# Optimization experiments

Hardware: AMD Instinct MI355X
Metric: run time of the kernel (lower is better)

Reference implementation:

```python
import jax, jax.numpy as jnp
import numpy as np

D_MODEL = 256
D_STATE = 64
D_CONV = 4
EXPAND = 2
HEADDIM = 64
D_INNER = EXPAND * D_MODEL            # 512
NHEADS = D_INNER // HEADDIM           # 8
D_XBC = D_INNER + 2 * D_STATE         # 640 (x, B, C; ngroups=1)
D_IN_PROJ = 2 * D_INNER + 2 * D_STATE + NHEADS  # 1160


def setup_inputs() -> dict:
    key = jax.random.key(0)
    ks = jax.random.split(key, 8)
    x = jax.random.normal(ks[0], (64, 5000, 12), jnp.float32)
    W_in = jax.random.normal(ks[1], (D_MODEL, D_IN_PROJ), jnp.float32) * 0.02
    conv_w = jax.random.normal(ks[2], (D_XBC, D_CONV), jnp.float32) * 0.1
    conv_b = jnp.zeros((D_XBC,), jnp.float32)
    A_log = jnp.log(jax.random.uniform(ks[3], (NHEADS,), jnp.float32, 1.0, 16.0))
    dt_bias = jax.random.normal(ks[4], (NHEADS,), jnp.float32) * 0.1
    D = jnp.ones((NHEADS,), jnp.float32)
    norm_w = jnp.ones((D_INNER,), jnp.float32)
    W_out = jax.random.normal(ks[5], (D_INNER, D_MODEL), jnp.float32) * 0.02
    return {"x": x, "W_in": W_in, "conv_w": conv_w, "conv_b": conv_b,
            "A_log": A_log, "dt_bias": dt_bias, "D": D,
            "norm_w": norm_w, "W_out": W_out}


def _mamba2(u, W_in, conv_w, conv_b, A_log, dt_bias, D, norm_w, W_out):
    b, l, _ = u.shape
    zxbcdt = u @ W_in                                   # (b,l,1160)
    z = zxbcdt[..., :D_INNER]                           # (b,l,512)
    xBC = zxbcdt[..., D_INNER:D_INNER + D_XBC]          # (b,l,640)
    dt = zxbcdt[..., D_INNER + D_XBC:]                  # (b,l,8)
    # causal depthwise conv1d (kernel 4) + SiLU
    xp = jnp.pad(xBC, ((0, 0), (D_CONV - 1, 0), (0, 0)))
    xBC = sum(xp[:, k:k + l, :] * conv_w[:, k] for k in range(D_CONV)) + conv_b
    xBC = jax.nn.silu(xBC)
    xs = xBC[..., :D_INNER].reshape(b, l, NHEADS, HEADDIM)
    Bm = xBC[..., D_INNER:D_INNER + D_STATE]            # (b,l,64)
    Cm = xBC[..., D_INNER + D_STATE:]                   # (b,l,64)
    dt = jax.nn.softplus(dt + dt_bias)                  # (b,l,h)
    A = -jnp.exp(A_log)                                 # (h,)

    def step(h, inp):
        x_t, dt_t, B_t, C_t = inp                       # (b,h,p),(b,h),(b,n),(b,n)
        decay = jnp.exp(dt_t * A)                       # (b,h)
        h = h * decay[..., None, None] + (dt_t[..., None] * x_t)[..., None] * B_t[:, None, None, :]
        y = jnp.einsum('bhpn,bn->bhp', h, C_t)
        return h, y

    h0 = jnp.zeros((b, NHEADS, HEADDIM, D_STATE), u.dtype)
    _, ys = jax.lax.scan(step, h0, (xs.transpose(1, 0, 2, 3), dt.transpose(1, 0, 2),
                                    Bm.transpose(1, 0, 2), Cm.transpose(1, 0, 2)))
    y = ys.transpose(1, 0, 2, 3) + D[None, None, :, None] * xs   # D skip, per head
    y = y.reshape(b, l, D_INNER)
    # RMSNormGated: gate then rmsnorm
    y = y * jax.nn.silu(z)
    y = y * jax.lax.rsqrt(jnp.mean(y * y, axis=-1, keepdims=True) + 1e-5) * norm_w
    return y @ W_out                                    # (b,l,256)


def reference(x, W_in, conv_w, conv_b, A_log, dt_bias, D, norm_w, W_out):
    b = x.shape[0]
    u = x.reshape(b, 250, 240)                          # 'b (t p1) f -> b t (p1 f)'
    u = jnp.pad(u, ((0, 0), (0, 0), (0, D_MODEL - 240)))
    y = _mamba2(u, W_in, conv_w, conv_b, A_log, dt_bias, D, norm_w, W_out)
    y = jax.nn.selu(y)                                  # AlphaDropout is identity at eval
    y = y[..., :240]
    return y.reshape(b, 5000, 12)
```

## Files before the change

kernel.cpp:

```cpp
#include <hip/hip_runtime.h>
#include <cstdint>
#include <cstddef>

#define D_MODEL 256
#define D_STATE 64
#define HEADDIM 64
#define D_INNER 512
#define NHEADS 8
#define D_XBC 640
#define NPROJ 1160
#define ZXW 1152
#define BATCH 64
#define SEQ 250
#define ROWS (BATCH * SEQ)
#define KIN 240
#define KPAD 256
#define NPAD 1280
#define TPAD 256

typedef __bf16 bf16x8 __attribute__((ext_vector_type(8)));
typedef float f32x4 __attribute__((ext_vector_type(4)));

typedef __attribute__((address_space(1))) const void gv_t;
typedef __attribute__((address_space(3))) void lv_t;

__device__ __forceinline__ float readlane_f(float v, int lane) {
    return __uint_as_float(__builtin_amdgcn_readlane(__float_as_uint(v), lane));
}
__device__ __forceinline__ float silu_f(float x) { return x * (1.f / (1.f + __expf(-x))); }
__device__ __forceinline__ unsigned short bf16_rne(float f) {
    unsigned int u = __float_as_uint(f);
    u += 0x7fff + ((u >> 16) & 1);
    return (unsigned short)(u >> 16);
}
__device__ __forceinline__ float bf2f(unsigned short u) {
    return __uint_as_float(((unsigned int)u) << 16);
}
__device__ __forceinline__ unsigned int pack2(float a, float b) {
    return (unsigned int)bf16_rne(a) | ((unsigned int)bf16_rne(b) << 16);
}

#define NA (ROWS * KPAD)
#define NB (NPAD * KPAD)
#define NW (D_MODEL * D_INNER)
__global__ __launch_bounds__(256) void cast_all_kernel(const float* __restrict__ x,
                                                       const float* __restrict__ Win,
                                                       const float* __restrict__ Wout,
                                                       unsigned short* __restrict__ a_bf,
                                                       unsigned short* __restrict__ bt_bf,
                                                       unsigned short* __restrict__ wt_bf) {
    int idx = blockIdx.x * 256 + threadIdx.x;
    if (idx < NA) {
        int row = idx >> 8, c = idx & 255;
        float v = (c < KIN) ? x[row * KIN + c] : 0.f;
        a_bf[idx] = bf16_rne(v);
    } else if (idx < NA + NB) {
        int r = idx - NA;
        int n = r >> 8, k = r & 255;
        float v = (n < NPROJ && k < KIN) ? Win[k * NPROJ + n] : 0.f;
        bt_bf[r] = bf16_rne(v);
    } else if (idx < NA + NB + NW) {
        int r = idx - NA - NB;
        int n = r & 255, k = r >> 8;
        wt_bf[n * D_INNER + k] = bf16_rne(Wout[k * D_MODEL + n]);
    }
}

__global__ __launch_bounds__(256) void gemm1_mfma(const unsigned short* __restrict__ A,
                                                  const unsigned short* __restrict__ Bt,
                                                  const float* __restrict__ dt_bias,
                                                  unsigned short* __restrict__ Czx,
                                                  float* __restrict__ dtp) {
    __shared__ unsigned short As[128 * 32];
    __shared__ unsigned short Bs[128 * 32];
    const int tid = threadIdx.x;
    const int lane = tid & 63, wave = tid >> 6;
    const int wm = wave >> 1, wn = wave & 1;
    const int q = lane >> 4, l15 = lane & 15;
    const int lin = blockIdx.y * 10 + blockIdx.x;
    const int xcd = lin & 7, rank = lin >> 3;
    const int newid = (xcd < 2 ? xcd * 157 : 2 * 157 + (xcd - 2) * 156) + rank;
    const int by = newid / 10, bx = newid - by * 10;
    const int rowBase = by * 128, colBase = bx * 128;
    f32x4 acc[4][4] = {};

    const int sr = tid >> 2;
    const int sc = (tid & 3) * 8;

    const unsigned short* gA = A + (size_t)(rowBase + sr) * KPAD + sc;
    const unsigned short* gB = Bt + (size_t)(colBase + sr) * KPAD + sc;
    unsigned short* lA = &As[sr * 32 + sc];
    unsigned short* lB = &Bs[sr * 32 + sc];

    for (int k0 = 0; k0 < KPAD; k0 += 32) {
        __builtin_amdgcn_global_load_lds((gv_t*)(gA + k0), (lv_t*)lA, 16, 0, 0);
        __builtin_amdgcn_global_load_lds((gv_t*)(gA + 64 * KPAD + k0),
                                         (lv_t*)(lA + 64 * 32), 16, 0, 0);
        __builtin_amdgcn_global_load_lds((gv_t*)(gB + k0), (lv_t*)lB, 16, 0, 0);
        __builtin_amdgcn_global_load_lds((gv_t*)(gB + 64 * KPAD + k0),
                                         (lv_t*)(lB + 64 * 32), 16, 0, 0);
        __syncthreads();

        bf16x8 bfr[4];
#pragma unroll
        for (int nt = 0; nt < 4; nt++)
            bfr[nt] = *(const bf16x8*)&Bs[(wn * 64 + nt * 16 + l15) * 32 + q * 8];
#pragma unroll
        for (int mt = 0; mt < 4; mt++) {
            bf16x8 afr = *(const bf16x8*)&As[(wm * 64 + mt * 16 + l15) * 32 + q * 8];
#pragma unroll
            for (int nt = 0; nt < 4; nt++)
                acc[mt][nt] = __builtin_amdgcn_mfma_f32_16x16x32_bf16(afr, bfr[nt],
                                                                      acc[mt][nt], 0, 0, 0);
        }
        __syncthreads();
    }
#pragma unroll
    for (int mt = 0; mt < 4; mt++) {
        int grow0 = rowBase + wm * 64 + mt * 16 + q * 4;
#pragma unroll
        for (int nt = 0; nt < 4; nt++) {
            int gcol = colBase + wn * 64 + nt * 16 + l15;
            if (gcol < ZXW) {
#pragma unroll
                for (int reg = 0; reg < 4; reg++) {
                    unsigned int u = bf16_rne(acc[mt][nt][reg]);
                    unsigned int partner = (unsigned int)__shfl_xor((int)u, 1, 64);
                    if ((l15 & 1) == 0)
                        *(unsigned int*)&Czx[(size_t)(grow0 + reg) * ZXW + gcol] =
                            u | (partner << 16);
                }
            } else if (gcol < NPROJ) {
                float bias = dt_bias[gcol - ZXW];
#pragma unroll
                for (int reg = 0; reg < 4; reg++) {
                    float v = acc[mt][nt][reg] + bias;
                    v = (v > 20.f) ? v : __logf(1.f + __expf(v));
                    dtp[(size_t)(grow0 + reg) * NHEADS + (gcol - ZXW)] = v;
                }
            }
        }
    }
}

#define CT_IN_STR 68
#define CT_TR_STR 70
__global__ __launch_bounds__(256) void conv_kernel(const unsigned short* __restrict__ zxbc,
                                                   const float* __restrict__ conv_w,
                                                   const float* __restrict__ conv_b,
                                                   unsigned short* __restrict__ xc_bf,
                                                   unsigned short* __restrict__ xcT_bf) {
    const int b = blockIdx.x;
    const int t0 = blockIdx.z * 64;
    __shared__ float In[67 * CT_IN_STR];
    __shared__ unsigned short OutT[64 * CT_TR_STR];
    const int cg = blockIdx.y;
    const int tid = threadIdx.x;
    const int lane = tid & 63;
    const int w = tid >> 6;
    const int ch = cg * 64 + lane;

    for (int r = w; r < 67; r += 4) {
        int t = t0 - 3 + r;
        float v = (t >= 0 && t < SEQ)
                      ? bf2f(zxbc[(size_t)(b * SEQ + t) * ZXW + D_INNER + ch])
                      : 0.f;
        In[r * CT_IN_STR + lane] = v;
    }
    __syncthreads();
    const float w0 = conv_w[ch * 4 + 0], w1 = conv_w[ch * 4 + 1];
    const float w2 = conv_w[ch * 4 + 2], w3 = conv_w[ch * 4 + 3];
    const float bias = conv_b[ch];
    unsigned short vals[16];
#pragma unroll
    for (int i = 0; i < 16; i++) {
        int tt = w * 16 + i;
        float acc = fmaf(w3, In[(tt + 3) * CT_IN_STR + lane],
                    fmaf(w2, In[(tt + 2) * CT_IN_STR + lane],
                    fmaf(w1, In[(tt + 1) * CT_IN_STR + lane],
                    fmaf(w0, In[tt * CT_IN_STR + lane], bias))));
        float sv = silu_f(acc);
        unsigned short bv = (t0 + tt < SEQ) ? bf16_rne(sv) : (unsigned short)0;
        vals[i] = bv;
        OutT[lane * CT_TR_STR + tt] = bv;
    }
    if (cg >= 8) {
#pragma unroll
        for (int i = 0; i < 16; i++) {
            int tt = w * 16 + i;
            if (t0 + tt < SEQ)
                xc_bf[(size_t)(b * SEQ + t0 + tt) * D_XBC + ch] = vals[i];
        }
    }
    if (cg <= 8) {
        __syncthreads();
        unsigned short* dstbase = xcT_bf + ((size_t)b * D_XBC + cg * 64) * TPAD + t0;
#pragma unroll
        for (int i = 0; i < 16; i++) {
            int c2 = w * 16 + i;
            dstbase[(size_t)c2 * TPAD + lane] = OutT[c2 * CT_TR_STR + lane];
        }
    }
}

#define LSTR 72
__global__ __launch_bounds__(256) void scan_fused(const unsigned short* __restrict__ xc_bf,
                                                  const unsigned short* __restrict__ xcT_bf,
                                                  const float* __restrict__ dtp,
                                                  const float* __restrict__ A_log,
                                                  const float* __restrict__ Dvec,
                                                  unsigned short* __restrict__ yout_bf) {
    __shared__ unsigned short C_l[64 * LSTR];
    __shared__ unsigned short BP_l[64 * LSTR];
    __shared__ unsigned short XT_l[64 * LSTR];
    __shared__ unsigned short H_l[64 * LSTR];
    __shared__ float cs_s[64], dts_s[64], fws_s[64];
    __shared__ float tot_s;

    const int bh = blockIdx.x;
    const int b = bh >> 3, h = bh & 7;
    const int tid = threadIdx.x;
    const int lane = tid & 63, w = tid >> 6;
    const int q = lane >> 4, l15 = lane & 15;
    const float A = -__expf(A_log[h]);
    const float Dh = Dvec[h];
    const int r = tid >> 2, c0 = (tid & 3) * 16;

    f32x4 h_acc[4] = {};

    float pdt0 = 0.f, pdt1 = 0.f, pdt2 = 0.f, pdt3 = 0.f;
    if (w == 0) {
        const float* dp = dtp + (size_t)(b * SEQ) * NHEADS + h;
        pdt0 = dp[(0 * 64 + lane) * NHEADS];
        pdt1 = dp[(1 * 64 + lane) * NHEADS];
        pdt2 = dp[(2 * 64 + lane) * NHEADS];
        if (192 + lane < SEQ) pdt3 = dp[(192 + lane) * NHEADS];
    }

    uint4 pC0, pC1, pB0, pB1, pX0, pX1, pbr0, pbr1;
    {
        const unsigned short* rowp = xc_bf + (size_t)(b * SEQ + r) * D_XBC;
        pC0 = *(const uint4*)&rowp[D_INNER + D_STATE + c0];
        pC1 = *(const uint4*)&rowp[D_INNER + D_STATE + c0 + 8];
        pB0 = *(const uint4*)&rowp[D_INNER + c0];
        pB1 = *(const uint4*)&rowp[D_INNER + c0 + 8];
        const unsigned short* xrow = xcT_bf + ((size_t)b * D_XBC + h * HEADDIM + r) * TPAD;
        pX0 = *(const uint4*)&xrow[c0];
        pX1 = *(const uint4*)&xrow[c0 + 8];
        const unsigned short* brow = xcT_bf + ((size_t)b * D_XBC + D_INNER + r) * TPAD + c0;
        pbr0 = *(const uint4*)&brow[0];
        pbr1 = *(const uint4*)&brow[8];
    }

    for (int c = 0; c < 4; ++c) {
        const int t0 = c * 64;
        if (c > 0) __syncthreads();

        *(uint4*)&C_l[r * LSTR + c0] = pC0;
        *(uint4*)&C_l[r * LSTR + c0 + 8] = pC1;
        *(uint4*)&BP_l[r * LSTR + c0] = pB0;
        *(uint4*)&BP_l[r * LSTR + c0 + 8] = pB1;
        *(uint4*)&XT_l[r * LSTR + c0] = pX0;
        *(uint4*)&XT_l[r * LSTR + c0 + 8] = pX1;
        const uint4 braw0 = pbr0, braw1 = pbr1;

        if (w == 0) {
            int t = lane;
            float dtv = (c == 0) ? pdt0 : (c == 1) ? pdt1 : (c == 2) ? pdt2 : pdt3;
            float csv = dtv * A;
#pragma unroll
            for (int o = 1; o < 64; o <<= 1) {
                float u = __shfl_up(csv, o, 64);
                if (lane >= o) csv += u;
            }
            float tot = readlane_f(csv, 63);
            cs_s[t] = csv;
            dts_s[t] = dtv;
            fws_s[t] = dtv * __expf(tot - csv);
            if (lane == 0) tot_s = tot;
        }
        __syncthreads();

        if (c < 3) {
            const int t1 = t0 + 64;
            if (t1 + r < SEQ) {
                const unsigned short* rowp = xc_bf + (size_t)(b * SEQ + t1 + r) * D_XBC;
                pC0 = *(const uint4*)&rowp[D_INNER + D_STATE + c0];
                pC1 = *(const uint4*)&rowp[D_INNER + D_STATE + c0 + 8];
                pB0 = *(const uint4*)&rowp[D_INNER + c0];
                pB1 = *(const uint4*)&rowp[D_INNER + c0 + 8];
            } else {
                uint4 z = {0, 0, 0, 0};
                pC0 = z; pC1 = z; pB0 = z; pB1 = z;
            }
            const unsigned short* xrow =
                xcT_bf + ((size_t)b * D_XBC + h * HEADDIM + r) * TPAD + t1;
            pX0 = *(const uint4*)&xrow[c0];
            pX1 = *(const uint4*)&xrow[c0 + 8];
            const unsigned short* brow =
                xcT_bf + ((size_t)b * D_XBC + D_INNER + r) * TPAD + t1 + c0;
            pbr0 = *(const uint4*)&brow[0];
            pbr1 = *(const uint4*)&brow[8];
        }

        f32x4 g[4] = {};
        f32x4 yi[4] = {};
#pragma unroll
        for (int k0 = 0; k0 < 64; k0 += 32) {
            bf16x8 ca = *(const bf16x8*)&C_l[(w * 16 + l15) * LSTR + k0 + q * 8];
#pragma unroll
            for (int nt = 0; nt < 4; nt++) {
                bf16x8 bb = *(const bf16x8*)&BP_l[(nt * 16 + l15) * LSTR + k0 + q * 8];
                g[nt] = __builtin_amdgcn_mfma_f32_16x16x32_bf16(ca, bb, g[nt], 0, 0, 0);
            }
            if (c > 0) {
#pragma unroll
                for (int nt = 0; nt < 4; nt++) {
                    bf16x8 hb = *(const bf16x8*)&H_l[(nt * 16 + l15) * LSTR + k0 + q * 8];
                    yi[nt] = __builtin_amdgcn_mfma_f32_16x16x32_bf16(ca, hb, yi[nt], 0, 0, 0);
                }
            }
        }
        __syncthreads();

        {
            unsigned short tmp[16];
            const unsigned short* rp = (const unsigned short*)&braw0;
#pragma unroll
            for (int j = 0; j < 8; j++) tmp[j] = bf16_rne(bf2f(rp[j]) * fws_s[c0 + j]);
            rp = (const unsigned short*)&braw1;
#pragma unroll
            for (int j = 0; j < 8; j++) tmp[8 + j] = bf16_rne(bf2f(rp[j]) * fws_s[c0 + 8 + j]);
            *(uint4*)&C_l[r * LSTR + c0] = *(uint4*)&tmp[0];
            *(uint4*)&C_l[r * LSTR + c0 + 8] = *(uint4*)&tmp[8];
        }
#pragma unroll
        for (int nt = 0; nt < 4; nt++) {
#pragma unroll
            for (int rr = 0; rr < 4; rr++) {
                int t = w * 16 + q * 4 + rr;
                int s = nt * 16 + l15;
                float pv = 0.f;
                if (s <= t) {
                    pv = g[nt][rr] * __expf(cs_s[t] - cs_s[s]) * dts_s[s];
                    if (s == t) pv += Dh;
                }
                unsigned int u = bf16_rne(pv);
                unsigned int partner = (unsigned int)__shfl_xor((int)u, 1, 64);
                if ((l15 & 1) == 0)
                    *(unsigned int*)&BP_l[t * LSTR + nt * 16 + l15] = u | (partner << 16);
            }
        }
        __syncthreads();

        f32x4 y[4] = {};
#pragma unroll
        for (int k0 = 0; k0 < 64; k0 += 32) {
            bf16x8 pa = *(const bf16x8*)&BP_l[(w * 16 + l15) * LSTR + k0 + q * 8];
#pragma unroll
            for (int nt = 0; nt < 4; nt++) {
                bf16x8 xb = *(const bf16x8*)&XT_l[(nt * 16 + l15) * LSTR + k0 + q * 8];
                y[nt] = __builtin_amdgcn_mfma_f32_16x16x32_bf16(pa, xb, y[nt], 0, 0, 0);
            }
        }
        if (c < 3) {
            f32x4 st[4] = {};
#pragma unroll
            for (int k0 = 0; k0 < 64; k0 += 32) {
                bf16x8 xa = *(const bf16x8*)&XT_l[(w * 16 + l15) * LSTR + k0 + q * 8];
#pragma unroll
                for (int nt = 0; nt < 4; nt++) {
                    bf16x8 bwb = *(const bf16x8*)&C_l[(nt * 16 + l15) * LSTR + k0 + q * 8];
                    st[nt] = __builtin_amdgcn_mfma_f32_16x16x32_bf16(xa, bwb, st[nt], 0, 0, 0);
                }
            }
            const float decay = __expf(tot_s);
#pragma unroll
            for (int nt = 0; nt < 4; nt++) {
                h_acc[nt] = st[nt] + decay * h_acc[nt];
#pragma unroll
                for (int rr = 0; rr < 4; rr++) {
                    unsigned int u = bf16_rne(h_acc[nt][rr]);
                    unsigned int partner = (unsigned int)__shfl_xor((int)u, 1, 64);
                    if ((l15 & 1) == 0)
                        *(unsigned int*)&H_l[(w * 16 + q * 4 + rr) * LSTR + nt * 16 + l15] =
                            u | (partner << 16);
                }
            }
        }
#pragma unroll
        for (int nt = 0; nt < 4; nt++)
#pragma unroll
            for (int rr = 0; rr < 4; rr++) {
                int t = w * 16 + q * 4 + rr;
                if (t0 + t < SEQ) {
                    int p = nt * 16 + l15;
                    float yv = y[nt][rr];
                    if (c > 0) yv += __expf(cs_s[t]) * yi[nt][rr];
                    unsigned int u = bf16_rne(yv);
                    unsigned int partner = (unsigned int)__shfl_xor((int)u, 1, 64);
                    if ((l15 & 1) == 0)
                        *(unsigned int*)&yout_bf[(size_t)(b * SEQ + t0 + t) * D_INNER +
                                                 h * HEADDIM + p] = u | (partner << 16);
                }
            }
    }
}

#define SA 40
__global__ __launch_bounds__(256) void gemm2_fused(const unsigned short* __restrict__ yout_bf,
                                                   const unsigned short* __restrict__ zxbc,
                                                   const unsigned short* __restrict__ Bt,
                                                   const float* __restrict__ norm_w,
                                                   float* __restrict__ out) {
    __shared__ unsigned short As2[32 * SA];
    __shared__ unsigned short Bs2[256 * SA];
    __shared__ float rms_s[32];
    const int tid = threadIdx.x;
    const int lane = tid & 63;
    const int wn = tid >> 6;
    const int q = lane >> 4, l15 = lane & 15;
    const int rowBase = blockIdx.x * 32;
    f32x4 acc[2][4] = {};

    const int tr = tid >> 3;
    const int tk = (tid & 7) * 4;

    const unsigned short* yrow = yout_bf + (size_t)(rowBase + tr) * D_INNER + tk;
    const unsigned short* zrow = zxbc + (size_t)(rowBase + tr) * ZXW + tk;
    float ssq = 0.f;

    for (int k0 = 0; k0 < D_INNER; k0 += 32) {
        uint2 yp = *(const uint2*)&yrow[k0];
        uint2 zp = *(const uint2*)&zrow[k0];
        float4 nw = *(const float4*)&norm_w[k0 + tk];
        const unsigned short* ys = (const unsigned short*)&yp;
        const unsigned short* zs = (const unsigned short*)&zp;
        float g0 = bf2f(ys[0]) * silu_f(bf2f(zs[0]));
        float g1 = bf2f(ys[1]) * silu_f(bf2f(zs[1]));
        float g2 = bf2f(ys[2]) * silu_f(bf2f(zs[2]));
        float g3 = bf2f(ys[3]) * silu_f(bf2f(zs[3]));
        ssq = fmaf(g0, g0, ssq);
        ssq = fmaf(g1, g1, ssq);
        ssq = fmaf(g2, g2, ssq);
        ssq = fmaf(g3, g3, ssq);
        uint2 pk;
        pk.x = pack2(g0 * nw.x, g1 * nw.y);
        pk.y = pack2(g2 * nw.z, g3 * nw.w);
        *(uint2*)&As2[tr * SA + tk] = pk;
        const unsigned short* brow = Bt + (size_t)tid * D_INNER + k0;
        *(uint4*)&Bs2[tid * SA + 0] = *(const uint4*)&brow[0];
        *(uint4*)&Bs2[tid * SA + 8] = *(const uint4*)&brow[8];
        *(uint4*)&Bs2[tid * SA + 16] = *(const uint4*)&brow[16];
        *(uint4*)&Bs2[tid * SA + 24] = *(const uint4*)&brow[24];
        __syncthreads();

        bf16x8 bfr[4];
#pragma unroll
        for (int nt = 0; nt < 4; nt++)
            bfr[nt] = *(const bf16x8*)&Bs2[(wn * 64 + nt * 16 + l15) * SA + q * 8];
#pragma unroll
        for (int mt = 0; mt < 2; mt++) {
            bf16x8 afr = *(const bf16x8*)&As2[(mt * 16 + l15) * SA + q * 8];
#pragma unroll
            for (int nt = 0; nt < 4; nt++)
                acc[mt][nt] = __builtin_amdgcn_mfma_f32_16x16x32_bf16(afr, bfr[nt],
                                                                      acc[mt][nt], 0, 0, 0);
        }
        __syncthreads();
    }
    ssq += __shfl_xor(ssq, 1, 64);
    ssq += __shfl_xor(ssq, 2, 64);
    ssq += __shfl_xor(ssq, 4, 64);
    if ((tid & 7) == 0) rms_s[tr] = rsqrtf(ssq * (1.f / 512.f) + 1e-5f);
    __syncthreads();

    const float SC = 1.0507009873554805f, AL = 1.6732632423543772f;
#pragma unroll
    for (int mt = 0; mt < 2; mt++) {
        int lrow0 = mt * 16 + q * 4;
#pragma unroll
        for (int nt = 0; nt < 4; nt++) {
            int gcol = wn * 64 + nt * 16 + l15;
            if (gcol < 240) {
#pragma unroll
                for (int reg = 0; reg < 4; reg++) {
                    float v = acc[mt][nt][reg] * rms_s[lrow0 + reg];
                    v = (v > 0.f) ? SC * v : SC * AL * (__expf(v) - 1.f);
                    out[(size_t)(rowBase + lrow0 + reg) * 240 + gcol] = v;
                }
            }
        }
    }
}

extern "C" void kernel_launch(void* const* d_in, const int* in_sizes, int n_in,
                              void* d_out, int out_size, void* d_ws, size_t ws_size,
                              hipStream_t stream) {
    const float* x = (const float*)d_in[0];
    const float* W_in = (const float*)d_in[1];
    const float* conv_w = (const float*)d_in[2];
    const float* conv_b = (const float*)d_in[3];
    const float* A_log = (const float*)d_in[4];
    const float* dt_bias = (const float*)d_in[5];
    const float* Dv = (const float*)d_in[6];
    const float* norm_w = (const float*)d_in[7];
    const float* W_out = (const float*)d_in[8];
    float* out = (float*)d_out;

    unsigned short* us = (unsigned short*)d_ws;
    unsigned short* zxbc_bf = us;
    unsigned short* xc_bf = zxbc_bf + (size_t)ROWS * ZXW;
    unsigned short* xcT_bf = xc_bf + (size_t)ROWS * D_XBC;
    unsigned short* yout_bf = xcT_bf + (size_t)BATCH * D_XBC * TPAD;
    unsigned short* bt_bf = yout_bf + (size_t)ROWS * D_INNER;
    unsigned short* wt_bf = bt_bf + (size_t)NPAD * KPAD;
    float* dtp = (float*)(wt_bf + (size_t)D_MODEL * D_INNER);
    unsigned short* a_bf = (unsigned short*)(dtp + (size_t)ROWS * NHEADS);

    int cast_total = NA + NB + NW;
    cast_all_kernel<<<dim3((cast_total + 255) / 256), 256, 0, stream>>>(x, W_in, W_out,
                                                                        a_bf, bt_bf, wt_bf);

    gemm1_mfma<<<dim3(NPAD / 128, ROWS / 128), 256, 0, stream>>>(a_bf, bt_bf, dt_bias,
                                                                 zxbc_bf, dtp);

    conv_kernel<<<dim3(BATCH, 10, 4), 256, 0, stream>>>(zxbc_bf, conv_w, conv_b,
                                                        xc_bf, xcT_bf);

    scan_fused<<<dim3(BATCH * NHEADS), 256, 0, stream>>>(xc_bf, xcT_bf, dtp, A_log, Dv,
                                                         yout_bf);

    gemm2_fused<<<dim3(ROWS / 32), 256, 0, stream>>>(yout_bf, zxbc_bf, wt_bf, norm_w, out);
}
```

Baseline: 189.5 us.

## Split scan block work across 8 waves with 2 N-tiles each

```diff
diff --git a/kernel.cpp b/kernel.cpp
--- a/kernel.cpp
+++ b/kernel.cpp
@@ -204,7 +204,7 @@
 }
 
 #define LSTR 72
-__global__ __launch_bounds__(256) void scan_fused(const unsigned short* __restrict__ xc_bf,
+__global__ __launch_bounds__(512) void scan_fused(const unsigned short* __restrict__ xc_bf,
                                                   const unsigned short* __restrict__ xcT_bf,
                                                   const float* __restrict__ dtp,
                                                   const float* __restrict__ A_log,
@@ -221,12 +221,15 @@
     const int b = bh >> 3, h = bh & 7;
     const int tid = threadIdx.x;
     const int lane = tid & 63, w = tid >> 6;
+    const int wt = w >> 1;
+    const int wn2 = w & 1;
     const int q = lane >> 4, l15 = lane & 15;
     const float A = -__expf(A_log[h]);
     const float Dh = Dvec[h];
-    const int r = tid >> 2, c0 = (tid & 3) * 16;
-
-    f32x4 h_acc[4] = {};
+    const int r = tid >> 3;
+    const int c0 = (tid & 7) * 8;
+
+    f32x4 h_acc[2] = {};
 
     float pdt0 = 0.f, pdt1 = 0.f, pdt2 = 0.f, pdt3 = 0.f;
     if (w == 0) {
@@ -237,32 +240,25 @@
         if (192 + lane < SEQ) pdt3 = dp[(192 + lane) * NHEADS];
     }
 
-    uint4 pC0, pC1, pB0, pB1, pX0, pX1, pbr0, pbr1;
+    uint4 pC, pB, pX, pbr;
     {
         const unsigned short* rowp = xc_bf + (size_t)(b * SEQ + r) * D_XBC;
-        pC0 = *(const uint4*)&rowp[D_INNER + D_STATE + c0];
-        pC1 = *(const uint4*)&rowp[D_INNER + D_STATE + c0 + 8];
-        pB0 = *(const uint4*)&rowp[D_INNER + c0];
-        pB1 = *(const uint4*)&rowp[D_INNER + c0 + 8];
+        pC = *(const uint4*)&rowp[D_INNER + D_STATE + c0];
+        pB = *(const uint4*)&rowp[D_INNER + c0];
         const unsigned short* xrow = xcT_bf + ((size_t)b * D_XBC + h * HEADDIM + r) * TPAD;
-        pX0 = *(const uint4*)&xrow[c0];
-        pX1 = *(const uint4*)&xrow[c0 + 8];
+        pX = *(const uint4*)&xrow[c0];
         const unsigned short* brow = xcT_bf + ((size_t)b * D_XBC + D_INNER + r) * TPAD + c0;
-        pbr0 = *(const uint4*)&brow[0];
-        pbr1 = *(const uint4*)&brow[8];
+        pbr = *(const uint4*)&brow[0];
     }
 
     for (int c = 0; c < 4; ++c) {
         const int t0 = c * 64;
         if (c > 0) __syncthreads();
 
-        *(uint4*)&C_l[r * LSTR + c0] = pC0;
-        *(uint4*)&C_l[r * LSTR + c0 + 8] = pC1;
-        *(uint4*)&BP_l[r * LSTR + c0] = pB0;
-        *(uint4*)&BP_l[r * LSTR + c0 + 8] = pB1;
-        *(uint4*)&XT_l[r * LSTR + c0] = pX0;
-        *(uint4*)&XT_l[r * LSTR + c0 + 8] = pX1;
-        const uint4 braw0 = pbr0, braw1 = pbr1;
+        *(uint4*)&C_l[r * LSTR + c0] = pC;
+        *(uint4*)&BP_l[r * LSTR + c0] = pB;
+        *(uint4*)&XT_l[r * LSTR + c0] = pX;
+        const uint4 braw = pbr;
 
         if (w == 0) {
             int t = lane;
@@ -285,64 +281,59 @@
             const int t1 = t0 + 64;
             if (t1 + r < SEQ) {
                 const unsigned short* rowp = xc_bf + (size_t)(b * SEQ + t1 + r) * D_XBC;
-                pC0 = *(const uint4*)&rowp[D_INNER + D_STATE + c0];
-                pC1 = *(const uint4*)&rowp[D_INNER + D_STATE + c0 + 8];
-                pB0 = *(const uint4*)&rowp[D_INNER + c0];
-                pB1 = *(const uint4*)&rowp[D_INNER + c0 + 8];
+                pC = *(const uint4*)&rowp[D_INNER + D_STATE + c0];
+                pB = *(const uint4*)&rowp[D_INNER + c0];
             } else {
                 uint4 z = {0, 0, 0, 0};
-                pC0 = z; pC1 = z; pB0 = z; pB1 = z;
+                pC = z; pB = z;
             }
             const unsigned short* xrow =
                 xcT_bf + ((size_t)b * D_XBC + h * HEADDIM + r) * TPAD + t1;
-            pX0 = *(const uint4*)&xrow[c0];
-            pX1 = *(const uint4*)&xrow[c0 + 8];
+            pX = *(const uint4*)&xrow[c0];
             const unsigned short* brow =
                 xcT_bf + ((size_t)b * D_XBC + D_INNER + r) * TPAD + t1 + c0;
-            pbr0 = *(const uint4*)&brow[0];
-            pbr1 = *(const uint4*)&brow[8];
-        }
-
-        f32x4 g[4] = {};
-        f32x4 yi[4] = {};
+            pbr = *(const uint4*)&brow[0];
+        }
+
+        f32x4 g[2] = {};
+        f32x4 yi[2] = {};
 #pragma unroll
         for (int k0 = 0; k0 < 64; k0 += 32) {
-            bf16x8 ca = *(const bf16x8*)&C_l[(w * 16 + l15) * LSTR + k0 + q * 8];
-#pragma unroll
-            for (int nt = 0; nt < 4; nt++) {
+            bf16x8 ca = *(const bf16x8*)&C_l[(wt * 16 + l15) * LSTR + k0 + q * 8];
+#pragma unroll
+            for (int j = 0; j < 2; j++) {
+                int nt = wn2 * 2 + j;
                 bf16x8 bb = *(const bf16x8*)&BP_l[(nt * 16 + l15) * LSTR + k0 + q * 8];
-                g[nt] = __builtin_amdgcn_mfma_f32_16x16x32_bf16(ca, bb, g[nt], 0, 0, 0);
+                g[j] = __builtin_amdgcn_mfma_f32_16x16x32_bf16(ca, bb, g[j], 0, 0, 0);
             }
             if (c > 0) {
 #pragma unroll
-                for (int nt = 0; nt < 4; nt++) {
+                for (int j = 0; j < 2; j++) {
+                    int nt = wn2 * 2 + j;
                     bf16x8 hb = *(const bf16x8*)&H_l[(nt * 16 + l15) * LSTR + k0 + q * 8];
-                    yi[nt] = __builtin_amdgcn_mfma_f32_16x16x32_bf16(ca, hb, yi[nt], 0, 0, 0);
+                    yi[j] = __builtin_amdgcn_mfma_f32_16x16x32_bf16(ca, hb, yi[j], 0, 0, 0);
                 }
             }
         }
         __syncthreads();
 
         {
-            unsigned short tmp[16];
-            const unsigned short* rp = (const unsigned short*)&braw0;
+            unsigned short tmp[8];
+            const unsigned short* rp = (const unsigned short*)&braw;
 #pragma unroll
             for (int j = 0; j < 8; j++) tmp[j] = bf16_rne(bf2f(rp[j]) * fws_s[c0 + j]);
-            rp = (const unsigned short*)&braw1;
-#pragma unroll
-            for (int j = 0; j < 8; j++) tmp[8 + j] = bf16_rne(bf2f(rp[j]) * fws_s[c0 + 8 + j]);
             *(uint4*)&C_l[r * LSTR + c0] = *(uint4*)&tmp[0];
-            *(uint4*)&C_l[r * LSTR + c0 + 8] = *(uint4*)&tmp[8];
-        }
-#pragma unroll
-        for (int nt = 0; nt < 4; nt++) {
+        }
+#pragma unroll
+        for (int j = 0; j < 2; j++) {
+            int nt = wn2 * 2 + j;
 #pragma unroll
             for (int rr = 0; rr < 4; rr++) {
-                int t = w * 16 + q * 4 + rr;
+                int t = wt * 16 + q * 4 + rr;
                 int s = nt * 16 + l15;
                 float pv = 0.f;
                 if (s <= t) {
-                    pv = g[nt][rr] * __expf(cs_s[t] - cs_s[s]) * dts_s[s];
+                    pv = g[j][rr] * __expf(cs_s[t] - cs_s[s]) * dts_s[s];
                     if (s == t) pv += Dh;
                 }
                 unsigned int u = bf16_rne(pv);
@@ -353,50 +344,54 @@
         }
         __syncthreads();
 
-        f32x4 y[4] = {};
+        f32x4 y[2] = {};
 #pragma unroll
         for (int k0 = 0; k0 < 64; k0 += 32) {
-            bf16x8 pa = *(const bf16x8*)&BP_l[(w * 16 + l15) * LSTR + k0 + q * 8];
-#pragma unroll
-            for (int nt = 0; nt < 4; nt++) {
+            bf16x8 pa = *(const bf16x8*)&BP_l[(wt * 16 + l15) * LSTR + k0 + q * 8];
+#pragma unroll
+            for (int j = 0; j < 2; j++) {
+                int nt = wn2 * 2 + j;
                 bf16x8 xb = *(const bf16x8*)&XT_l[(nt * 16 + l15) * LSTR + k0 + q * 8];
-                y[nt] = __builtin_amdgcn_mfma_f32_16x16x32_bf16(pa, xb, y[nt], 0, 0, 0);
+                y[j] = __builtin_amdgcn_mfma_f32_16x16x32_bf16(pa, xb, y[j], 0, 0, 0);
             }
         }
         if (c < 3) {
-            f32x4 st[4] = {};
+            f32x4 st[2] = {};
 #pragma unroll
             for (int k0 = 0; k0 < 64; k0 += 32) {
-                bf16x8 xa = *(const bf16x8*)&XT_l[(w * 16 + l15) * LSTR + k0 + q * 8];
-#pragma unroll
-                for (int nt = 0; nt < 4; nt++) {
+                bf16x8 xa = *(const bf16x8*)&XT_l[(wt * 16 + l15) * LSTR + k0 + q * 8];
+#pragma unroll
+                for (int j = 0; j < 2; j++) {
+                    int nt = wn2 * 2 + j;
                     bf16x8 bwb = *(const bf16x8*)&C_l[(nt * 16 + l15) * LSTR + k0 + q * 8];
-                    st[nt] = __builtin_amdgcn_mfma_f32_16x16x32_bf16(xa, bwb, st[nt], 0, 0, 0);
+                    st[j] = __builtin_amdgcn_mfma_f32_16x16x32_bf16(xa, bwb, st[j], 0, 0, 0);
                 }
             }
             const float decay = __expf(tot_s);
 #pragma unroll
-            for (int nt = 0; nt < 4; nt++) {
-                h_acc[nt] = st[nt] + decay * h_acc[nt];
+            for (int j = 0; j < 2; j++) {
+                int nt = wn2 * 2 + j;
+                h_acc[j] = st[j] + decay * h_acc[j];
 #pragma unroll
                 for (int rr = 0; rr < 4; rr++) {
-                    unsigned int u = bf16_rne(h_acc[nt][rr]);
+                    unsigned int u = bf16_rne(h_acc[j][rr]);
                     unsigned int partner = (unsigned int)__shfl_xor((int)u, 1, 64);
                     if ((l15 & 1) == 0)
-                        *(unsigned int*)&H_l[(w * 16 + q * 4 + rr) * LSTR + nt * 16 + l15] =
+                        *(unsigned int*)&H_l[(wt * 16 + q * 4 + rr) * LSTR + nt * 16 + l15] =
                             u | (partner << 16);
                 }
             }
         }
 #pragma unroll
-        for (int nt = 0; nt < 4; nt++)
+        for (int j = 0; j < 2; j++) {
+            int nt = wn2 * 2 + j;
 #pragma unroll
             for (int rr = 0; rr < 4; rr++) {
-                int t = w * 16 + q * 4 + rr;
+                int t = wt * 16 + q * 4 + rr;
                 if (t0 + t < SEQ) {
                     int p = nt * 16 + l15;
-                    float yv = y[nt][rr];
-                    if (c > 0) yv += __expf(cs_s[t]) * yi[nt][rr];
+                    float yv = y[j][rr];
+                    if (c > 0) yv += __expf(cs_s[t]) * yi[j][rr];
                     unsigned int u = bf16_rne(yv);
                     unsigned int partner = (unsigned int)__shfl_xor((int)u, 1, 64);
                     if ((l15 & 1) == 0)
@@ -404,6 +399,7 @@
                                                  h * HEADDIM + p] = u | (partner << 16);
                 }
             }
+        }
     }
 }
 
@@ -528,7 +524,7 @@
     conv_kernel<<<dim3(BATCH, 10, 4), 256, 0, stream>>>(zxbc_bf, conv_w, conv_b,
                                                         xc_bf, xcT_bf);
 
-    scan_fused<<<dim3(BATCH * NHEADS), 256, 0, stream>>>(xc_bf, xcT_bf, dtp, A_log, Dv,
+    scan_fused<<<dim3(BATCH * NHEADS), 512, 0, stream>>>(xc_bf, xcT_bf, dtp, A_log, Dv,
                                                          yout_bf);
 
     gemm2_fused<<<dim3(ROWS / 32), 256, 0, stream>>>(yout_bf, zxbc_bf, wt_bf, norm_w, out);
```

Measured after the change: 180.8 us. 1.05x faster.
